# Optimization experiments

Hardware: AMD Instinct MI355X
Metric: run time of the kernel (lower is better)

Reference implementation:

```python
import jax, jax.numpy as jnp
import numpy as np

VOCAB, EMBED, HIDDEN, N_LAYER, TAG = 32000, 512, 1024, 2, 10
BATCH, MAXLEN, PAD_ID = 64, 512, 0


def setup_inputs() -> dict:
    key = jax.random.key(0)
    ks = jax.random.split(key, 12)
    x = jax.random.randint(ks[0], (BATCH, MAXLEN), 0, VOCAB, dtype=jnp.int64 if jax.config.jax_enable_x64 else jnp.int32)
    emb = jax.random.normal(ks[1], (VOCAB, EMBED), dtype=jnp.float32) * 0.02
    emb = emb.at[PAD_ID].set(0.0)  # padding_idx row zeroed
    s = 1.0 / np.sqrt(HIDDEN)
    def u(k, shape):
        return jax.random.uniform(k, shape, jnp.float32, -s, s)
    # layer 0: input EMBED -> HIDDEN; layer 1: HIDDEN -> HIDDEN. Gate order i,f,g,o.
    W_ih0 = u(ks[2], (4 * HIDDEN, EMBED))
    W_hh0 = u(ks[3], (4 * HIDDEN, HIDDEN))
    b0 = u(ks[4], (4 * HIDDEN,)) + u(ks[5], (4 * HIDDEN,))  # b_ih + b_hh fused
    W_ih1 = u(ks[6], (4 * HIDDEN, HIDDEN))
    W_hh1 = u(ks[7], (4 * HIDDEN, HIDDEN))
    b1 = u(ks[8], (4 * HIDDEN,)) + u(ks[9], (4 * HIDDEN,))
    W_out = u(ks[10], (TAG, HIDDEN))
    b_out = u(ks[11], (TAG,))
    return {"x": x, "emb": emb, "W_ih0": W_ih0, "W_hh0": W_hh0, "b0": b0,
            "W_ih1": W_ih1, "W_hh1": W_hh1, "b1": b1, "W_out": W_out, "b_out": b_out}


def lstm_layer(seq, W_ih, W_hh, b):
    # seq: [B, T, D] -> [B, T, H]
    B = seq.shape[0]
    H = W_hh.shape[1]
    x_proj = jnp.einsum('btd,gd->btg', seq, W_ih) + b  # [B, T, 4H] input projection precomputed
    x_proj = jnp.swapaxes(x_proj, 0, 1)  # [T, B, 4H]

    def step(carry, xp):
        h, c = carry
        gates = xp + h @ W_hh.T  # [B, 4H]
        i, f, g, o = jnp.split(gates, 4, axis=-1)
        c = jax.nn.sigmoid(f) * c + jax.nn.sigmoid(i) * jnp.tanh(g)
        h = jax.nn.sigmoid(o) * jnp.tanh(c)
        return (h, c), h

    init = (jnp.zeros((B, H), seq.dtype), jnp.zeros((B, H), seq.dtype))
    _, hs = jax.lax.scan(step, init, x_proj)  # hs: [T, B, H]
    return jnp.swapaxes(hs, 0, 1)


def reference(x, emb, W_ih0, W_hh0, b0, W_ih1, W_hh1, b1, W_out, b_out):
    B, T = x.shape
    lens = T - (x == PAD_ID).sum(axis=-1)  # cal_seq_len
    h = emb[x]  # [B, T, EMBED]
    h = lstm_layer(h, W_ih0, W_hh0, b0)
    h = lstm_layer(h, W_ih1, W_hh1, b1)
    last = h[jnp.arange(B), lens - 1, :]  # gather last valid hidden state
    return last @ W_out.T + b_out  # [B, TAG]
```

## Files before the change

kernel.cpp:

```cpp
#include <hip/hip_runtime.h>
#include <stdint.h>

#define BB 64
#define TT 512
#define EE 512
#define HH 1024
#define GG 4096

#define NSG 64
#define XP0_SLOTS 8

typedef short v8b __attribute__((ext_vector_type(8)));
typedef float v4f __attribute__((ext_vector_type(4)));
typedef unsigned short u16;
typedef unsigned int u32;
typedef unsigned long long u64;

__device__ __forceinline__ u16 f2bf(float f) {
  union { float f; u32 i; } v; v.f = f;
  u32 u = v.i;
  return (u16)((u + 0x7FFFu + ((u >> 16) & 1u)) >> 16);
}
__device__ __forceinline__ float sigm(float x) { return 1.0f / (1.0f + __expf(-x)); }
__device__ __forceinline__ float ftanh(float x) {
  float e = __expf(2.0f * x);
  return 1.0f - 2.0f / (e + 1.0f);
}

__device__ __forceinline__ u64 ld8a(const void* p) {
  return __hip_atomic_load((const u64*)p, __ATOMIC_RELAXED, __HIP_MEMORY_SCOPE_AGENT);
}
__device__ __forceinline__ v4f ldf16a(const float* p) {
  union { v4f f; u64 q[2]; } u;
  u.q[0] = ld8a((const u64*)p);
  u.q[1] = ld8a((const u64*)p + 1);
  return u.f;
}
__device__ __forceinline__ void stg16_f(float* p, v4f v) {
  union { v4f f; u64 q[2]; } u; u.f = v;
  __hip_atomic_store((u64*)p,     u.q[0], __ATOMIC_RELAXED, __HIP_MEMORY_SCOPE_AGENT);
  __hip_atomic_store((u64*)p + 1, u.q[1], __ATOMIC_RELAXED, __HIP_MEMORY_SCOPE_AGENT);
}
__device__ __forceinline__ void stg2_h(u16* p, u16 v) {
  __hip_atomic_store(p, v, __ATOMIC_RELAXED, __HIP_MEMORY_SCOPE_AGENT);
}
__device__ __forceinline__ void stg4_f(float* p, float v) {
  __hip_atomic_store(p, v, __ATOMIC_RELAXED, __HIP_MEMORY_SCOPE_AGENT);
}
__device__ __forceinline__ void drain_stores() {
  asm volatile("s_waitcnt vmcnt(0)" ::: "memory");
}

__device__ __forceinline__ u32 ldflag(const u32* p) {
  return __hip_atomic_load(p, __ATOMIC_RELAXED, __HIP_MEMORY_SCOPE_AGENT);
}
__device__ __forceinline__ void spin3(const u32* p0, u32 v0,
                                      const u32* p1, u32 v1,
                                      const u32* p2, u32 v2) {
  for (;;) {
    bool ok = (ldflag(p0) >= v0) && (ldflag(p1) >= v1) && (ldflag(p2) >= v2);
    if (__all((int)ok)) break;
    __builtin_amdgcn_s_sleep(1);
  }
}
__device__ __forceinline__ void postw(u32* f, u32 v, int lane) {
  if (lane == 0)
    __hip_atomic_store(f, v, __ATOMIC_RELAXED, __HIP_MEMORY_SCOPE_AGENT);
}

__global__ void prep_kernel(const int* __restrict__ x, const float* __restrict__ emb,
                            u16* __restrict__ e16, u16* __restrict__ h0r, u16* __restrict__ h1r,
                            int* __restrict__ lens, u32* flags, int flag_u32s) {
  long stride = (long)gridDim.x * blockDim.x;
  long gid = (long)blockIdx.x * blockDim.x + threadIdx.x;
  const long totalE = (long)BB * TT * EE;
  for (long i = gid; i < totalE; i += stride) {
    int d = (int)(i % EE);
    long bt = i / EE;
    int tok = x[bt];
    e16[i] = f2bf(emb[(long)tok * EE + d]);
  }
  for (long i = gid; i < (long)flag_u32s; i += stride) flags[i] = 0u;
  const long ringN = 4L * BB * HH;
  for (long i = gid; i < ringN; i += stride) { h0r[i] = 0; h1r[i] = 0; }
  int gwave = (int)(gid >> 6);
  int lane = (int)(gid & 63);
  if (gwave < BB) {
    int cnt = 0;
    for (int t2 = lane; t2 < TT; t2 += 64) cnt += (x[gwave * TT + t2] == 0) ? 1 : 0;
    for (int off = 32; off; off >>= 1) cnt += __shfl_down(cnt, off, 64);
    if (lane == 0) lens[gwave] = TT - cnt;
  }
}

extern __shared__ short Wlds[];

#define KQUAD(FR, PK) \
  { const short* wb = &Wlds[(((PK) * 4 + q) * 64 + m16) * 8]; \
    v8b w0 = *(const v8b*)(wb); \
    v8b w1 = *(const v8b*)(wb + 128); \
    v8b w2 = *(const v8b*)(wb + 256); \
    v8b w3 = *(const v8b*)(wb + 384); \
    a0 = __builtin_amdgcn_mfma_f32_16x16x32_bf16(FR, w0, a0, 0, 0, 0); \
    a1 = __builtin_amdgcn_mfma_f32_16x16x32_bf16(FR, w1, a1, 0, 0, 0); \
    a2 = __builtin_amdgcn_mfma_f32_16x16x32_bf16(FR, w2, a2, 0, 0, 0); \
    a3 = __builtin_amdgcn_mfma_f32_16x16x32_bf16(FR, w3, a3, 0, 0, 0); }

__device__ __forceinline__ void kh_staged(const u16* hbase ,
                                          int lbase ,
                                          int lane, int q, int m16,
                                          v4f& a0, v4f& a1, v4f& a2, v4f& a3) {
  const int lrow = lane >> 4;
  const int lcol = lane & 15;
  const int wG = lcol >> 1;
  const int wH = lane & 1;
  u64 hh[64];
#pragma unroll
  for (int c = 0; c < 16; ++c) {
#pragma unroll
    for (int j = 0; j < 4; ++j) {
      const u16* p = hbase + (long)(lrow + 4 * j) * HH + c * 64;
      hh[c * 4 + j] = ld8a((const u64*)p + lcol);
    }
  }
#pragma unroll
  for (int j = 0; j < 4; ++j) {
    int r = lrow + 4 * j;
    int Gs = wG ^ (r & 7);
    *(u64*)&Wlds[lbase + r * 64 + Gs * 8 + wH * 4] = hh[j];
  }
#pragma unroll
  for (int c = 0; c < 16; ++c) {
    const int boff = lbase + (c & 1) * 1024;
#pragma unroll
    for (int kb = 0; kb < 2; ++kb) {
      int Gs = (q + 4 * kb) ^ (m16 & 7);
      v8b fr = *(const v8b*)&Wlds[boff + m16 * 64 + Gs * 8];
      KQUAD(fr, c * 2 + kb);
    }
    if (c < 15) {
      const int woff = lbase + ((c + 1) & 1) * 1024;
#pragma unroll
      for (int j = 0; j < 4; ++j) {
        int r = lrow + 4 * j;
        int Gs = wG ^ (r & 7);
        *(u64*)&Wlds[woff + r * 64 + Gs * 8 + wH * 4] = hh[(c + 1) * 4 + j];
      }
    }
  }
}

__global__ __launch_bounds__(256, 1) void lstm_persist(
    const u16* __restrict__ e16,
    const float* __restrict__ Wih0, const float* __restrict__ Whh0, const float* __restrict__ b0,
    const float* __restrict__ Wih1, const float* __restrict__ Whh1, const float* __restrict__ b1,
    const int* __restrict__ lens,
    float* __restrict__ xp0, float* __restrict__ xp1,
    u16* __restrict__ h0r, u16* __restrict__ h1r,
    float* __restrict__ lasth,
    u32* fA0, u32* fL0, u32* fA1, u32* fL1) {
  const int wg = blockIdx.x;
  const int tid = threadIdx.x;
  const int g = tid >> 6;
  const int lane = tid & 63;
  const int m16 = lane & 15;
  const int q = lane >> 4;
  const int bq = g * 16 + q * 4;
  const int stage = wg >> 6;
  const int sid = wg & 63;
  const int lbase = 65536 + g * 2048;

  if (stage == 0) {
    const int rbase = sid * 64;
    for (int c2 = tid; c2 < 64 * 64; c2 += 256) {
      int r = c2 >> 6, kb = c2 & 63;
      const float* src = Wih0 + (long)(rbase + r) * EE + kb * 8;
      v8b w;
#pragma unroll
      for (int j = 0; j < 8; ++j) w[j] = (short)f2bf(src[j]);
      *(v8b*)&Wlds[(kb * 64 + r) * 8] = w;
    }
    __syncthreads();
    float bias[4];
#pragma unroll
    for (int nt = 0; nt < 4; ++nt) bias[nt] = b0[rbase + nt * 16 + m16];
    const u32* cf = fL0 + g * 64 + (sid & 15) * 4 + (lane & 3);
    u32* myf = fA0 + g * 64 + sid;
    for (int t = 0; t < TT; ++t) {
      u32 need = (t >= XP0_SLOTS) ? (u32)(t - XP0_SLOTS + 1) : 0u;
      spin3(cf, need, cf, 0u, cf, 0u);
      v4f a0 = {0,0,0,0}, a1 = {0,0,0,0}, a2 = {0,0,0,0}, a3 = {0,0,0,0};
      const u16* ap = e16 + (long)(g * 16 + m16) * (TT * EE) + (long)t * EE + q * 8;
#pragma unroll
      for (int kb = 0; kb < 16; ++kb) {
        v8b fr = *(const v8b*)(ap + kb * 32);
        KQUAD(fr, kb);
      }
      float* xpS = xp0 + (long)(t & (XP0_SLOTS - 1)) * (GG * BB);
      stg16_f(&xpS[(long)(rbase + 0 * 16 + m16) * BB + bq], a0 + bias[0]);
      stg16_f(&xpS[(long)(rbase + 1 * 16 + m16) * BB + bq], a1 + bias[1]);
      stg16_f(&xpS[(long)(rbase + 2 * 16 + m16) * BB + bq], a2 + bias[2]);
      stg16_f(&xpS[(long)(rbase + 3 * 16 + m16) * BB + bq], a3 + bias[3]);
      drain_stores();
      postw(myf, (u32)(t + 1), lane);
    }
  } else if (stage == 1) {
    const int ubase = sid * 16;
    for (int c2 = tid; c2 < 64 * 128; c2 += 256) {
      int r = c2 >> 7, kb = c2 & 127;
      int grow = (r >> 4) * HH + ubase + (r & 15);
      const float* src = Whh0 + (long)grow * HH + kb * 8;
      v8b w;
#pragma unroll
      for (int j = 0; j < 8; ++j) w[j] = (short)f2bf(src[j]);
      *(v8b*)&Wlds[(kb * 64 + r) * 8] = w;
    }
    __syncthreads();
    float cst[4] = {0.f, 0.f, 0.f, 0.f};
    const u32* fa = fA0 + g * 64 + ((lane & 3) << 4) + (sid >> 2);
    const u32* fp = fL0 + g * 64 + lane;
    const u32* fr_ = fA1 + g * 64 + lane;
    u32* myf = fL0 + g * 64 + sid;
    for (int t = 0; t < TT; ++t) {
      spin3(fa, (u32)(t + 1), fp, (u32)t, fr_, (t >= 4) ? (u32)(t - 3) : 0u);
      const float* xpS = xp0 + (long)(t & (XP0_SLOTS - 1)) * (GG * BB);
      v4f xq0 = ldf16a(&xpS[(long)(0 * HH + ubase + m16) * BB + bq]);
      v4f xq1 = ldf16a(&xpS[(long)(1 * HH + ubase + m16) * BB + bq]);
      v4f xq2 = ldf16a(&xpS[(long)(2 * HH + ubase + m16) * BB + bq]);
      v4f xq3 = ldf16a(&xpS[(long)(3 * HH + ubase + m16) * BB + bq]);
      v4f a0 = {0,0,0,0}, a1 = {0,0,0,0}, a2 = {0,0,0,0}, a3 = {0,0,0,0};
      const u16* hb = h0r + ((t + 3) & 3) * (BB * HH) + (long)(g * 16) * HH;
      kh_staged(hb, lbase, lane, q, m16, a0, a1, a2, a3);
      a0 += xq0; a1 += xq1; a2 += xq2; a3 += xq3;
      u16* hw = h0r + (t & 3) * (BB * HH);
#pragma unroll
      for (int r = 0; r < 4; ++r) {
        float cn = sigm(a1[r]) * cst[r] + sigm(a0[r]) * ftanh(a2[r]);
        cst[r] = cn;
        float hv = sigm(a3[r]) * ftanh(cn);
        stg2_h(&hw[(bq + r) * HH + ubase + m16], f2bf(hv));
      }
      drain_stores();
      postw(myf, (u32)(t + 1), lane);
    }
  } else if (stage == 2) {
    const int rbase = sid * 64;
    for (int c2 = tid; c2 < 64 * 128; c2 += 256) {
      int r = c2 >> 7, kb = c2 & 127;
      const float* src = Wih1 + (long)(rbase + r) * HH + kb * 8;
      v8b w;
#pragma unroll
      for (int j = 0; j < 8; ++j) w[j] = (short)f2bf(src[j]);
      *(v8b*)&Wlds[(kb * 64 + r) * 8] = w;
    }
    __syncthreads();
    float bias[4];
#pragma unroll
    for (int nt = 0; nt < 4; ++nt) bias[nt] = b1[rbase + nt * 16 + m16];
    const u32* fp = fL0 + g * 64 + lane;
    const u32* fc = fL1 + g * 64 + (sid & 15) * 4 + (lane & 3);
    u32* myf = fA1 + g * 64 + sid;
    for (int t = 0; t < TT; ++t) {
      spin3(fp, (u32)(t + 1), fc, (t >= 4) ? (u32)(t - 3) : 0u, fp, 0u);
      v4f a0 = {0,0,0,0}, a1 = {0,0,0,0}, a2 = {0,0,0,0}, a3 = {0,0,0,0};
      const u16* hb = h0r + (t & 3) * (BB * HH) + (long)(g * 16) * HH;
      kh_staged(hb, lbase, lane, q, m16, a0, a1, a2, a3);
      float* xpS = xp1 + (long)(t & 3) * (GG * BB);
      stg16_f(&xpS[(long)(rbase + 0 * 16 + m16) * BB + bq], a0 + bias[0]);
      stg16_f(&xpS[(long)(rbase + 1 * 16 + m16) * BB + bq], a1 + bias[1]);
      stg16_f(&xpS[(long)(rbase + 2 * 16 + m16) * BB + bq], a2 + bias[2]);
      stg16_f(&xpS[(long)(rbase + 3 * 16 + m16) * BB + bq], a3 + bias[3]);
      drain_stores();
      postw(myf, (u32)(t + 1), lane);
    }
  } else {
    const int ubase = sid * 16;
    for (int c2 = tid; c2 < 64 * 128; c2 += 256) {
      int r = c2 >> 7, kb = c2 & 127;
      int grow = (r >> 4) * HH + ubase + (r & 15);
      const float* src = Whh1 + (long)grow * HH + kb * 8;
      v8b w;
#pragma unroll
      for (int j = 0; j < 8; ++j) w[j] = (short)f2bf(src[j]);
      *(v8b*)&Wlds[(kb * 64 + r) * 8] = w;
    }
    __syncthreads();
    float cst[4] = {0.f, 0.f, 0.f, 0.f};
    int cap[4];
#pragma unroll
    for (int r = 0; r < 4; ++r) {
      int l = lens[bq + r];
      cap[r] = (l > 0) ? (l - 1) : (TT - 1);
    }
    const u32* fa = fA1 + g * 64 + ((lane & 3) << 4) + (sid >> 2);
    const u32* fp = fL1 + g * 64 + lane;
    u32* myf = fL1 + g * 64 + sid;
    for (int t = 0; t < TT; ++t) {
      spin3(fa, (u32)(t + 1), fp, (u32)t, fa, 0u);
      const float* xpS = xp1 + (long)(t & 3) * (GG * BB);
      v4f xq0 = ldf16a(&xpS[(long)(0 * HH + ubase + m16) * BB + bq]);
      v4f xq1 = ldf16a(&xpS[(long)(1 * HH + ubase + m16) * BB + bq]);
      v4f xq2 = ldf16a(&xpS[(long)(2 * HH + ubase + m16) * BB + bq]);
      v4f xq3 = ldf16a(&xpS[(long)(3 * HH + ubase + m16) * BB + bq]);
      v4f a0 = {0,0,0,0}, a1 = {0,0,0,0}, a2 = {0,0,0,0}, a3 = {0,0,0,0};
      const u16* hb = h1r + ((t + 3) & 3) * (BB * HH) + (long)(g * 16) * HH;
      kh_staged(hb, lbase, lane, q, m16, a0, a1, a2, a3);
      a0 += xq0; a1 += xq1; a2 += xq2; a3 += xq3;
      u16* hw = h1r + (t & 3) * (BB * HH);
#pragma unroll
      for (int r = 0; r < 4; ++r) {
        float cn = sigm(a1[r]) * cst[r] + sigm(a0[r]) * ftanh(a2[r]);
        cst[r] = cn;
        float hv = sigm(a3[r]) * ftanh(cn);
        stg2_h(&hw[(bq + r) * HH + ubase + m16], f2bf(hv));
        if (t == cap[r]) stg4_f(&lasth[(long)(bq + r) * HH + ubase + m16], hv);
      }
      drain_stores();
      postw(myf, (u32)(t + 1), lane);
    }
  }
}

__global__ void out_kernel(const float* __restrict__ lasth, const float* __restrict__ Wout,
                           const float* __restrict__ bout, float* __restrict__ out) {
  int b = blockIdx.x;
  int k = threadIdx.x;
  if (k < 10) {
    float acc = bout[k];
    const float* hb = lasth + (long)b * HH;
    const float* wr = Wout + (long)k * HH;
    for (int j = 0; j < HH; ++j) acc += hb[j] * wr[j];
    out[b * 10 + k] = acc;
  }
}

extern "C" void kernel_launch(void* const* d_in, const int* in_sizes, int n_in,
                              void* d_out, int out_size, void* d_ws, size_t ws_size,
                              hipStream_t stream) {
  const int*   x    = (const int*)d_in[0];
  const float* emb  = (const float*)d_in[1];
  const float* Wih0 = (const float*)d_in[2];
  const float* Whh0 = (const float*)d_in[3];
  const float* b0   = (const float*)d_in[4];
  const float* Wih1 = (const float*)d_in[5];
  const float* Whh1 = (const float*)d_in[6];
  const float* b1   = (const float*)d_in[7];
  const float* Wout = (const float*)d_in[8];
  const float* bout = (const float*)d_in[9];

  char* ws = (char*)d_ws;
  u16*   e16   = (u16*)(ws + 0);
  float* xp0   = (float*)(ws + 33554432);
  float* xp1   = (float*)(ws + 41943040);
  u16*   h0r   = (u16*)(ws + 46137344);
  u16*   h1r   = (u16*)(ws + 46661632);
  float* lasth = (float*)(ws + 47185920);
  int*   lens  = (int*)(ws + 47448064);
  u32*   flags = (u32*)(ws + 47448320);
  u32* fA0 = flags;
  u32* fL0 = fA0 + 4 * NSG;
  u32* fA1 = fL0 + 4 * NSG;
  u32* fL1 = fA1 + 4 * NSG;
  int flag_u32s = 16 * NSG;

  (void)hipFuncSetAttribute((const void*)lstm_persist,
                            hipFuncAttributeMaxDynamicSharedMemorySize, 147456);

  prep_kernel<<<2048, 256, 0, stream>>>(x, emb, e16, h0r, h1r, lens, flags, flag_u32s);
  lstm_persist<<<4 * NSG, 256, 147456, stream>>>(e16, Wih0, Whh0, b0, Wih1, Whh1, b1, lens,
                                                 xp0, xp1, h0r, h1r, lasth, fA0, fL0, fA1, fL1);
  out_kernel<<<BB, 64, 0, stream>>>(lasth, Wout, bout, (float*)d_out);
}
```

Baseline: 5.167 ms.

## Load h fragments directly into MFMA operands and pack h stores via LDS

Replaces the LDS-staged hidden-state loading (load to registers, write swizzled to LDS, read back fragments) with direct 16-byte atomic global loads into MFMA A-operands, double-buffered in two register banks of eight fragments. The 2-byte per-element h stores are replaced by an LDS exchange that packs four bf16 values into one 8-byte global store per lane. The spin-wait helpers are split by flag count so redundant flag polls are dropped, and the dynamic LDS size shrinks. This removes LDS round trips and store count on the serial recurrent critical path, at the cost of more global load traffic and register pressure.

```diff
diff --git a/kernel.cpp b/kernel.cpp
--- a/kernel.cpp
+++ b/kernel.cpp
@@ -30,6 +30,12 @@
 __device__ __forceinline__ u64 ld8a(const void* p) {
   return __hip_atomic_load((const u64*)p, __ATOMIC_RELAXED, __HIP_MEMORY_SCOPE_AGENT);
 }
+__device__ __forceinline__ v8b ld16a(const u16* p) {
+  union { v8b b; u64 q[2]; } u;
+  u.q[0] = ld8a(p);
+  u.q[1] = ld8a(p + 4);
+  return u.b;
+}
 __device__ __forceinline__ v4f ldf16a(const float* p) {
   union { v4f f; u64 q[2]; } u;
   u.q[0] = ld8a((const u64*)p);
@@ -41,8 +47,8 @@
   __hip_atomic_store((u64*)p,     u.q[0], __ATOMIC_RELAXED, __HIP_MEMORY_SCOPE_AGENT);
   __hip_atomic_store((u64*)p + 1, u.q[1], __ATOMIC_RELAXED, __HIP_MEMORY_SCOPE_AGENT);
 }
-__device__ __forceinline__ void stg2_h(u16* p, u16 v) {
-  __hip_atomic_store(p, v, __ATOMIC_RELAXED, __HIP_MEMORY_SCOPE_AGENT);
+__device__ __forceinline__ void stg8(void* p, u64 v) {
+  __hip_atomic_store((u64*)p, v, __ATOMIC_RELAXED, __HIP_MEMORY_SCOPE_AGENT);
 }
 __device__ __forceinline__ void stg4_f(float* p, float v) {
   __hip_atomic_store(p, v, __ATOMIC_RELAXED, __HIP_MEMORY_SCOPE_AGENT);
@@ -50,15 +56,38 @@
 __device__ __forceinline__ void drain_stores() {
   asm volatile("s_waitcnt vmcnt(0)" ::: "memory");
 }
+__device__ __forceinline__ void lds_fence() {
+  asm volatile("s_waitcnt lgkmcnt(0)" ::: "memory");
+}
 
 __device__ __forceinline__ u32 ldflag(const u32* p) {
   return __hip_atomic_load(p, __ATOMIC_RELAXED, __HIP_MEMORY_SCOPE_AGENT);
 }
-__device__ __forceinline__ void spin3(const u32* p0, u32 v0,
-                                      const u32* p1, u32 v1,
-                                      const u32* p2, u32 v2) {
+__device__ __forceinline__ void spin1p(const u32* p0, u32 v0) {
   for (;;) {
-    bool ok = (ldflag(p0) >= v0) && (ldflag(p1) >= v1) && (ldflag(p2) >= v2);
+    u32 a = ldflag(p0);
+    if (__all((int)(a >= v0))) break;
+    __builtin_amdgcn_s_sleep(1);
+  }
+}
+__device__ __forceinline__ void spin2p(const u32* p0, u32 v0,
+                                       const u32* p1, u32 v1) {
+  for (;;) {
+    u32 a = ldflag(p0);
+    u32 b = ldflag(p1);
+    bool ok = (a >= v0) & (b >= v1);
+    if (__all((int)ok)) break;
+    __builtin_amdgcn_s_sleep(1);
+  }
+}
+__device__ __forceinline__ void spin3p(const u32* p0, u32 v0,
+                                       const u32* p1, u32 v1,
+                                       const u32* p2, u32 v2) {
+  for (;;) {
+    u32 a = ldflag(p0);
+    u32 b = ldflag(p1);
+    u32 c = ldflag(p2);
+    bool ok = (a >= v0) & (b >= v1) & (c >= v2);
     if (__all((int)ok)) break;
     __builtin_amdgcn_s_sleep(1);
   }
@@ -106,48 +135,25 @@
     a2 = __builtin_amdgcn_mfma_f32_16x16x32_bf16(FR, w2, a2, 0, 0, 0); \
     a3 = __builtin_amdgcn_mfma_f32_16x16x32_bf16(FR, w3, a3, 0, 0, 0); }
 
-__device__ __forceinline__ void kh_staged(const u16* hbase ,
-                                          int lbase ,
-                                          int lane, int q, int m16,
-                                          v4f& a0, v4f& a1, v4f& a2, v4f& a3) {
-  const int lrow = lane >> 4;
-  const int lcol = lane & 15;
-  const int wG = lcol >> 1;
-  const int wH = lane & 1;
-  u64 hh[64];
-#pragma unroll
-  for (int c = 0; c < 16; ++c) {
-#pragma unroll
-    for (int j = 0; j < 4; ++j) {
-      const u16* p = hbase + (long)(lrow + 4 * j) * HH + c * 64;
-      hh[c * 4 + j] = ld8a((const u64*)p + lcol);
-    }
-  }
-#pragma unroll
-  for (int j = 0; j < 4; ++j) {
-    int r = lrow + 4 * j;
-    int Gs = wG ^ (r & 7);
-    *(u64*)&Wlds[lbase + r * 64 + Gs * 8 + wH * 4] = hh[j];
-  }
-#pragma unroll
-  for (int c = 0; c < 16; ++c) {
-    const int boff = lbase + (c & 1) * 1024;
-#pragma unroll
-    for (int kb = 0; kb < 2; ++kb) {
-      int Gs = (q + 4 * kb) ^ (m16 & 7);
-      v8b fr = *(const v8b*)&Wlds[boff + m16 * 64 + Gs * 8];
-      KQUAD(fr, c * 2 + kb);
-    }
-    if (c < 15) {
-      const int woff = lbase + ((c + 1) & 1) * 1024;
-#pragma unroll
-      for (int j = 0; j < 4; ++j) {
-        int r = lrow + 4 * j;
-        int Gs = wG ^ (r & 7);
-        *(u64*)&Wlds[woff + r * 64 + Gs * 8 + wH * 4] = hh[(c + 1) * 4 + j];
-      }
-    }
-  }
+__device__ __forceinline__ void khloop(const u16* hp, int q, int m16,
+                                       v4f& a0, v4f& a1, v4f& a2, v4f& a3) {
+  v8b A[8], B[8];
+#pragma unroll
+  for (int i = 0; i < 8; ++i) A[i] = ld16a(hp + i * 32);
+#pragma unroll
+  for (int i = 0; i < 8; ++i) B[i] = ld16a(hp + (8 + i) * 32);
+#pragma unroll
+  for (int i = 0; i < 8; ++i) KQUAD(A[i], i);
+#pragma unroll
+  for (int i = 0; i < 8; ++i) A[i] = ld16a(hp + (16 + i) * 32);
+#pragma unroll
+  for (int i = 0; i < 8; ++i) KQUAD(B[i], 8 + i);
+#pragma unroll
+  for (int i = 0; i < 8; ++i) B[i] = ld16a(hp + (24 + i) * 32);
+#pragma unroll
+  for (int i = 0; i < 8; ++i) KQUAD(A[i], 16 + i);
+#pragma unroll
+  for (int i = 0; i < 8; ++i) KQUAD(B[i], 24 + i);
 }
 
 __global__ __launch_bounds__(256, 1) void lstm_persist(
@@ -168,7 +174,7 @@
   const int bq = g * 16 + q * 4;
   const int stage = wg >> 6;
   const int sid = wg & 63;
-  const int lbase = 65536 + g * 2048;
+  const int exbase = 65536 + g * 256;
 
   if (stage == 0) {
     const int rbase = sid * 64;
@@ -187,8 +193,7 @@
     const u32* cf = fL0 + g * 64 + (sid & 15) * 4 + (lane & 3);
     u32* myf = fA0 + g * 64 + sid;
     for (int t = 0; t < TT; ++t) {
-      u32 need = (t >= XP0_SLOTS) ? (u32)(t - XP0_SLOTS + 1) : 0u;
-      spin3(cf, need, cf, 0u, cf, 0u);
+      if (t >= XP0_SLOTS) spin1p(cf, (u32)(t - XP0_SLOTS + 1));
       v4f a0 = {0,0,0,0}, a1 = {0,0,0,0}, a2 = {0,0,0,0}, a3 = {0,0,0,0};
       const u16* ap = e16 + (long)(g * 16 + m16) * (TT * EE) + (long)t * EE + q * 8;
 #pragma unroll
@@ -221,25 +226,30 @@
     const u32* fp = fL0 + g * 64 + lane;
     const u32* fr_ = fA1 + g * 64 + lane;
     u32* myf = fL0 + g * 64 + sid;
+    short* ex = &Wlds[exbase];
+    const int bl = lane >> 2, qa = lane & 3;
     for (int t = 0; t < TT; ++t) {
-      spin3(fa, (u32)(t + 1), fp, (u32)t, fr_, (t >= 4) ? (u32)(t - 3) : 0u);
+      spin3p(fa, (u32)(t + 1), fp, (u32)t, fr_, (t >= 4) ? (u32)(t - 3) : 0u);
       const float* xpS = xp0 + (long)(t & (XP0_SLOTS - 1)) * (GG * BB);
       v4f xq0 = ldf16a(&xpS[(long)(0 * HH + ubase + m16) * BB + bq]);
       v4f xq1 = ldf16a(&xpS[(long)(1 * HH + ubase + m16) * BB + bq]);
       v4f xq2 = ldf16a(&xpS[(long)(2 * HH + ubase + m16) * BB + bq]);
       v4f xq3 = ldf16a(&xpS[(long)(3 * HH + ubase + m16) * BB + bq]);
       v4f a0 = {0,0,0,0}, a1 = {0,0,0,0}, a2 = {0,0,0,0}, a3 = {0,0,0,0};
-      const u16* hb = h0r + ((t + 3) & 3) * (BB * HH) + (long)(g * 16) * HH;
-      kh_staged(hb, lbase, lane, q, m16, a0, a1, a2, a3);
+      const u16* hp = h0r + ((t + 3) & 3) * (BB * HH) + (long)(g * 16 + m16) * HH + q * 8;
+      khloop(hp, q, m16, a0, a1, a2, a3);
       a0 += xq0; a1 += xq1; a2 += xq2; a3 += xq3;
-      u16* hw = h0r + (t & 3) * (BB * HH);
 #pragma unroll
       for (int r = 0; r < 4; ++r) {
         float cn = sigm(a1[r]) * cst[r] + sigm(a0[r]) * ftanh(a2[r]);
         cst[r] = cn;
         float hv = sigm(a3[r]) * ftanh(cn);
-        stg2_h(&hw[(bq + r) * HH + ubase + m16], f2bf(hv));
+        ex[(q * 4 + r) * 16 + m16] = (short)f2bf(hv);
       }
+      lds_fence();
+      u16* hw = h0r + (t & 3) * (BB * HH);
+      u64 pk = *(const u64*)&ex[bl * 16 + qa * 4];
+      stg8(&hw[(long)(g * 16 + bl) * HH + ubase + qa * 4], pk);
       drain_stores();
       postw(myf, (u32)(t + 1), lane);
     }
@@ -261,10 +271,10 @@
     const u32* fc = fL1 + g * 64 + (sid & 15) * 4 + (lane & 3);
     u32* myf = fA1 + g * 64 + sid;
     for (int t = 0; t < TT; ++t) {
-      spin3(fp, (u32)(t + 1), fc, (t >= 4) ? (u32)(t - 3) : 0u, fp, 0u);
+      spin2p(fp, (u32)(t + 1), fc, (t >= 4) ? (u32)(t - 3) : 0u);
       v4f a0 = {0,0,0,0}, a1 = {0,0,0,0}, a2 = {0,0,0,0}, a3 = {0,0,0,0};
-      const u16* hb = h0r + (t & 3) * (BB * HH) + (long)(g * 16) * HH;
-      kh_staged(hb, lbase, lane, q, m16, a0, a1, a2, a3);
+      const u16* hp = h0r + (t & 3) * (BB * HH) + (long)(g * 16 + m16) * HH + q * 8;
+      khloop(hp, q, m16, a0, a1, a2, a3);
       float* xpS = xp1 + (long)(t & 3) * (GG * BB);
       stg16_f(&xpS[(long)(rbase + 0 * 16 + m16) * BB + bq], a0 + bias[0]);
       stg16_f(&xpS[(long)(rbase + 1 * 16 + m16) * BB + bq], a1 + bias[1]);
@@ -295,26 +305,31 @@
     const u32* fa = fA1 + g * 64 + ((lane & 3) << 4) + (sid >> 2);
     const u32* fp = fL1 + g * 64 + lane;
     u32* myf = fL1 + g * 64 + sid;
+    short* ex = &Wlds[exbase];
+    const int bl = lane >> 2, qa = lane & 3;
     for (int t = 0; t < TT; ++t) {
-      spin3(fa, (u32)(t + 1), fp, (u32)t, fa, 0u);
+      spin2p(fa, (u32)(t + 1), fp, (u32)t);
       const float* xpS = xp1 + (long)(t & 3) * (GG * BB);
       v4f xq0 = ldf16a(&xpS[(long)(0 * HH + ubase + m16) * BB + bq]);
       v4f xq1 = ldf16a(&xpS[(long)(1 * HH + ubase + m16) * BB + bq]);
       v4f xq2 = ldf16a(&xpS[(long)(2 * HH + ubase + m16) * BB + bq]);
       v4f xq3 = ldf16a(&xpS[(long)(3 * HH + ubase + m16) * BB + bq]);
       v4f a0 = {0,0,0,0}, a1 = {0,0,0,0}, a2 = {0,0,0,0}, a3 = {0,0,0,0};
-      const u16* hb = h1r + ((t + 3) & 3) * (BB * HH) + (long)(g * 16) * HH;
-      kh_staged(hb, lbase, lane, q, m16, a0, a1, a2, a3);
+      const u16* hp = h1r + ((t + 3) & 3) * (BB * HH) + (long)(g * 16 + m16) * HH + q * 8;
+      khloop(hp, q, m16, a0, a1, a2, a3);
       a0 += xq0; a1 += xq1; a2 += xq2; a3 += xq3;
-      u16* hw = h1r + (t & 3) * (BB * HH);
 #pragma unroll
       for (int r = 0; r < 4; ++r) {
         float cn = sigm(a1[r]) * cst[r] + sigm(a0[r]) * ftanh(a2[r]);
         cst[r] = cn;
         float hv = sigm(a3[r]) * ftanh(cn);
-        stg2_h(&hw[(bq + r) * HH + ubase + m16], f2bf(hv));
+        ex[(q * 4 + r) * 16 + m16] = (short)f2bf(hv);
         if (t == cap[r]) stg4_f(&lasth[(long)(bq + r) * HH + ubase + m16], hv);
       }
+      lds_fence();
+      u16* hw = h1r + (t & 3) * (BB * HH);
+      u64 pk = *(const u64*)&ex[bl * 16 + qa * 4];
+      stg8(&hw[(long)(g * 16 + bl) * HH + ubase + qa * 4], pk);
       drain_stores();
       postw(myf, (u32)(t + 1), lane);
     }
@@ -364,10 +379,10 @@
   int flag_u32s = 16 * NSG;
 
   (void)hipFuncSetAttribute((const void*)lstm_persist,
-                            hipFuncAttributeMaxDynamicSharedMemorySize, 147456);
+                            hipFuncAttributeMaxDynamicSharedMemorySize, 133120);
 
   prep_kernel<<<2048, 256, 0, stream>>>(x, emb, e16, h0r, h1r, lens, flags, flag_u32s);
-  lstm_persist<<<4 * NSG, 256, 147456, stream>>>(e16, Wih0, Whh0, b0, Wih1, Whh1, b1, lens,
+  lstm_persist<<<4 * NSG, 256, 133120, stream>>>(e16, Wih0, Whh0, b0, Wih1, Whh1, b1, lens,
                                                  xp0, xp1, h0r, h1r, lasth, fA0, fL0, fA1, fL1);
   out_kernel<<<BB, 64, 0, stream>>>(lasth, Wout, bout, (float*)d_out);
 }
```

Result: slower. 8.781 ms (+69.9%).

## Load recurrent h fragments directly from global, drop LDS staging, deepen rings

Applied to the files above, without the earlier changes.

Replaces the LDS-staged hidden-state load, which did coalesced 8-byte atomic loads, swizzled writes to shared memory and then read MFMA fragments back, with 16-byte global loads using sc0 sc1 cache bits that go straight into MFMA operand registers. The xproj loads use the same instruction. The h and xp1 ring buffers grow from 4 to 8 slots so producer stages can run further ahead, and the stage-0 spin is skipped for the first slots. This removes LDS traffic and per-step staging latency in the serial recurrence, at the cost of less coalesced global loads, higher register pressure (32 v8b fragments), and relying on inline-asm cache bits for cross-workgroup coherence.

```diff
diff --git a/kernel.cpp b/kernel.cpp
--- a/kernel.cpp
+++ b/kernel.cpp
@@ -9,6 +9,7 @@
 
 #define NSG 64
 #define XP0_SLOTS 8
+#define RS 8
 
 typedef short v8b __attribute__((ext_vector_type(8)));
 typedef float v4f __attribute__((ext_vector_type(4)));
@@ -27,15 +28,21 @@
   return 1.0f - 2.0f / (e + 1.0f);
 }
 
-__device__ __forceinline__ u64 ld8a(const void* p) {
-  return __hip_atomic_load((const u64*)p, __ATOMIC_RELAXED, __HIP_MEMORY_SCOPE_AGENT);
-}
-__device__ __forceinline__ v4f ldf16a(const float* p) {
-  union { v4f f; u64 q[2]; } u;
-  u.q[0] = ld8a((const u64*)p);
-  u.q[1] = ld8a((const u64*)p + 1);
-  return u.f;
-}
+__device__ __forceinline__ v8b ld16cc(const u16* p) {
+  v8b r;
+  asm volatile("global_load_dwordx4 %0, %1, off sc0 sc1" : "=v"(r) : "v"(p));
+  return r;
+}
+__device__ __forceinline__ v4f ldf16cc(const float* p) {
+  v4f r;
+  asm volatile("global_load_dwordx4 %0, %1, off sc0 sc1" : "=v"(r) : "v"(p));
+  return r;
+}
+__device__ __forceinline__ void wait_loads() {
+  asm volatile("s_waitcnt vmcnt(0)" ::: "memory");
+  __builtin_amdgcn_sched_barrier(0);
+}
+
 __device__ __forceinline__ void stg16_f(float* p, v4f v) {
   union { v4f f; u64 q[2]; } u; u.f = v;
   __hip_atomic_store((u64*)p,     u.q[0], __ATOMIC_RELAXED, __HIP_MEMORY_SCOPE_AGENT);
@@ -81,7 +88,7 @@
     e16[i] = f2bf(emb[(long)tok * EE + d]);
   }
   for (long i = gid; i < (long)flag_u32s; i += stride) flags[i] = 0u;
-  const long ringN = 4L * BB * HH;
+  const long ringN = (long)RS * BB * HH;
   for (long i = gid; i < ringN; i += stride) { h0r[i] = 0; h1r[i] = 0; }
   int gwave = (int)(gid >> 6);
   int lane = (int)(gid & 63);
@@ -106,48 +113,16 @@
     a2 = __builtin_amdgcn_mfma_f32_16x16x32_bf16(FR, w2, a2, 0, 0, 0); \
     a3 = __builtin_amdgcn_mfma_f32_16x16x32_bf16(FR, w3, a3, 0, 0, 0); }
 
-__device__ __forceinline__ void kh_staged(const u16* hbase ,
-                                          int lbase ,
-                                          int lane, int q, int m16,
+__device__ __forceinline__ void kh_direct(const u16* hbase ,
+                                          int q, int m16,
                                           v4f& a0, v4f& a1, v4f& a2, v4f& a3) {
-  const int lrow = lane >> 4;
-  const int lcol = lane & 15;
-  const int wG = lcol >> 1;
-  const int wH = lane & 1;
-  u64 hh[64];
-#pragma unroll
-  for (int c = 0; c < 16; ++c) {
-#pragma unroll
-    for (int j = 0; j < 4; ++j) {
-      const u16* p = hbase + (long)(lrow + 4 * j) * HH + c * 64;
-      hh[c * 4 + j] = ld8a((const u64*)p + lcol);
-    }
-  }
-#pragma unroll
-  for (int j = 0; j < 4; ++j) {
-    int r = lrow + 4 * j;
-    int Gs = wG ^ (r & 7);
-    *(u64*)&Wlds[lbase + r * 64 + Gs * 8 + wH * 4] = hh[j];
-  }
-#pragma unroll
-  for (int c = 0; c < 16; ++c) {
-    const int boff = lbase + (c & 1) * 1024;
-#pragma unroll
-    for (int kb = 0; kb < 2; ++kb) {
-      int Gs = (q + 4 * kb) ^ (m16 & 7);
-      v8b fr = *(const v8b*)&Wlds[boff + m16 * 64 + Gs * 8];
-      KQUAD(fr, c * 2 + kb);
-    }
-    if (c < 15) {
-      const int woff = lbase + ((c + 1) & 1) * 1024;
-#pragma unroll
-      for (int j = 0; j < 4; ++j) {
-        int r = lrow + 4 * j;
-        int Gs = wG ^ (r & 7);
-        *(u64*)&Wlds[woff + r * 64 + Gs * 8 + wH * 4] = hh[(c + 1) * 4 + j];
-      }
-    }
-  }
+  const u16* hp = hbase + (long)m16 * HH + q * 8;
+  v8b H[32];
+#pragma unroll
+  for (int kb = 0; kb < 32; ++kb) H[kb] = ld16cc(hp + kb * 32);
+  wait_loads();
+#pragma unroll
+  for (int kb = 0; kb < 32; ++kb) KQUAD(H[kb], kb);
 }
 
 __global__ __launch_bounds__(256, 1) void lstm_persist(
@@ -168,7 +143,6 @@
   const int bq = g * 16 + q * 4;
   const int stage = wg >> 6;
   const int sid = wg & 63;
-  const int lbase = 65536 + g * 2048;
 
   if (stage == 0) {
     const int rbase = sid * 64;
@@ -187,8 +161,7 @@
     const u32* cf = fL0 + g * 64 + (sid & 15) * 4 + (lane & 3);
     u32* myf = fA0 + g * 64 + sid;
     for (int t = 0; t < TT; ++t) {
-      u32 need = (t >= XP0_SLOTS) ? (u32)(t - XP0_SLOTS + 1) : 0u;
-      spin3(cf, need, cf, 0u, cf, 0u);
+      if (t >= XP0_SLOTS) spin3(cf, (u32)(t - XP0_SLOTS + 1), cf, 0u, cf, 0u);
       v4f a0 = {0,0,0,0}, a1 = {0,0,0,0}, a2 = {0,0,0,0}, a3 = {0,0,0,0};
       const u16* ap = e16 + (long)(g * 16 + m16) * (TT * EE) + (long)t * EE + q * 8;
 #pragma unroll
@@ -222,17 +195,17 @@
     const u32* fr_ = fA1 + g * 64 + lane;
     u32* myf = fL0 + g * 64 + sid;
     for (int t = 0; t < TT; ++t) {
-      spin3(fa, (u32)(t + 1), fp, (u32)t, fr_, (t >= 4) ? (u32)(t - 3) : 0u);
+      spin3(fa, (u32)(t + 1), fp, (u32)t, fr_, (t >= RS) ? (u32)(t - RS + 1) : 0u);
       const float* xpS = xp0 + (long)(t & (XP0_SLOTS - 1)) * (GG * BB);
-      v4f xq0 = ldf16a(&xpS[(long)(0 * HH + ubase + m16) * BB + bq]);
-      v4f xq1 = ldf16a(&xpS[(long)(1 * HH + ubase + m16) * BB + bq]);
-      v4f xq2 = ldf16a(&xpS[(long)(2 * HH + ubase + m16) * BB + bq]);
-      v4f xq3 = ldf16a(&xpS[(long)(3 * HH + ubase + m16) * BB + bq]);
+      v4f xq0 = ldf16cc(&xpS[(long)(0 * HH + ubase + m16) * BB + bq]);
+      v4f xq1 = ldf16cc(&xpS[(long)(1 * HH + ubase + m16) * BB + bq]);
+      v4f xq2 = ldf16cc(&xpS[(long)(2 * HH + ubase + m16) * BB + bq]);
+      v4f xq3 = ldf16cc(&xpS[(long)(3 * HH + ubase + m16) * BB + bq]);
       v4f a0 = {0,0,0,0}, a1 = {0,0,0,0}, a2 = {0,0,0,0}, a3 = {0,0,0,0};
-      const u16* hb = h0r + ((t + 3) & 3) * (BB * HH) + (long)(g * 16) * HH;
-      kh_staged(hb, lbase, lane, q, m16, a0, a1, a2, a3);
+      const u16* hb = h0r + ((t + RS - 1) & (RS - 1)) * (BB * HH) + (long)(g * 16) * HH;
+      kh_direct(hb, q, m16, a0, a1, a2, a3);
       a0 += xq0; a1 += xq1; a2 += xq2; a3 += xq3;
-      u16* hw = h0r + (t & 3) * (BB * HH);
+      u16* hw = h0r + (t & (RS - 1)) * (BB * HH);
 #pragma unroll
       for (int r = 0; r < 4; ++r) {
         float cn = sigm(a1[r]) * cst[r] + sigm(a0[r]) * ftanh(a2[r]);
@@ -261,11 +234,11 @@
     const u32* fc = fL1 + g * 64 + (sid & 15) * 4 + (lane & 3);
     u32* myf = fA1 + g * 64 + sid;
     for (int t = 0; t < TT; ++t) {
-      spin3(fp, (u32)(t + 1), fc, (t >= 4) ? (u32)(t - 3) : 0u, fp, 0u);
+      spin3(fp, (u32)(t + 1), fc, (t >= RS) ? (u32)(t - RS + 1) : 0u, fp, 0u);
       v4f a0 = {0,0,0,0}, a1 = {0,0,0,0}, a2 = {0,0,0,0}, a3 = {0,0,0,0};
-      const u16* hb = h0r + (t & 3) * (BB * HH) + (long)(g * 16) * HH;
-      kh_staged(hb, lbase, lane, q, m16, a0, a1, a2, a3);
-      float* xpS = xp1 + (long)(t & 3) * (GG * BB);
+      const u16* hb = h0r + (t & (RS - 1)) * (BB * HH) + (long)(g * 16) * HH;
+      kh_direct(hb, q, m16, a0, a1, a2, a3);
+      float* xpS = xp1 + (long)(t & (RS - 1)) * (GG * BB);
       stg16_f(&xpS[(long)(rbase + 0 * 16 + m16) * BB + bq], a0 + bias[0]);
       stg16_f(&xpS[(long)(rbase + 1 * 16 + m16) * BB + bq], a1 + bias[1]);
       stg16_f(&xpS[(long)(rbase + 2 * 16 + m16) * BB + bq], a2 + bias[2]);
@@ -297,16 +270,16 @@
     u32* myf = fL1 + g * 64 + sid;
     for (int t = 0; t < TT; ++t) {
       spin3(fa, (u32)(t + 1), fp, (u32)t, fa, 0u);
-      const float* xpS = xp1 + (long)(t & 3) * (GG * BB);
-      v4f xq0 = ldf16a(&xpS[(long)(0 * HH + ubase + m16) * BB + bq]);
-      v4f xq1 = ldf16a(&xpS[(long)(1 * HH + ubase + m16) * BB + bq]);
-      v4f xq2 = ldf16a(&xpS[(long)(2 * HH + ubase + m16) * BB + bq]);
-      v4f xq3 = ldf16a(&xpS[(long)(3 * HH + ubase + m16) * BB + bq]);
+      const float* xpS = xp1 + (long)(t & (RS - 1)) * (GG * BB);
+      v4f xq0 = ldf16cc(&xpS[(long)(0 * HH + ubase + m16) * BB + bq]);
+      v4f xq1 = ldf16cc(&xpS[(long)(1 * HH + ubase + m16) * BB + bq]);
+      v4f xq2 = ldf16cc(&xpS[(long)(2 * HH + ubase + m16) * BB + bq]);
+      v4f xq3 = ldf16cc(&xpS[(long)(3 * HH + ubase + m16) * BB + bq]);
       v4f a0 = {0,0,0,0}, a1 = {0,0,0,0}, a2 = {0,0,0,0}, a3 = {0,0,0,0};
-      const u16* hb = h1r + ((t + 3) & 3) * (BB * HH) + (long)(g * 16) * HH;
-      kh_staged(hb, lbase, lane, q, m16, a0, a1, a2, a3);
+      const u16* hb = h1r + ((t + RS - 1) & (RS - 1)) * (BB * HH) + (long)(g * 16) * HH;
+      kh_direct(hb, q, m16, a0, a1, a2, a3);
       a0 += xq0; a1 += xq1; a2 += xq2; a3 += xq3;
-      u16* hw = h1r + (t & 3) * (BB * HH);
+      u16* hw = h1r + (t & (RS - 1)) * (BB * HH);
 #pragma unroll
       for (int r = 0; r < 4; ++r) {
         float cn = sigm(a1[r]) * cst[r] + sigm(a0[r]) * ftanh(a2[r]);
@@ -352,11 +325,11 @@
   u16*   e16   = (u16*)(ws + 0);
   float* xp0   = (float*)(ws + 33554432);
   float* xp1   = (float*)(ws + 41943040);
-  u16*   h0r   = (u16*)(ws + 46137344);
-  u16*   h1r   = (u16*)(ws + 46661632);
-  float* lasth = (float*)(ws + 47185920);
-  int*   lens  = (int*)(ws + 47448064);
-  u32*   flags = (u32*)(ws + 47448320);
+  u16*   h0r   = (u16*)(ws + 50331648);
+  u16*   h1r   = (u16*)(ws + 51380224);
+  float* lasth = (float*)(ws + 52428800);
+  int*   lens  = (int*)(ws + 52690944);
+  u32*   flags = (u32*)(ws + 52691200);
   u32* fA0 = flags;
   u32* fL0 = fA0 + 4 * NSG;
   u32* fA1 = fL0 + 4 * NSG;
@@ -364,10 +337,10 @@
   int flag_u32s = 16 * NSG;
 
   (void)hipFuncSetAttribute((const void*)lstm_persist,
-                            hipFuncAttributeMaxDynamicSharedMemorySize, 147456);
+                            hipFuncAttributeMaxDynamicSharedMemorySize, 131072);
 
   prep_kernel<<<2048, 256, 0, stream>>>(x, emb, e16, h0r, h1r, lens, flags, flag_u32s);
-  lstm_persist<<<4 * NSG, 256, 147456, stream>>>(e16, Wih0, Whh0, b0, Wih1, Whh1, b1, lens,
+  lstm_persist<<<4 * NSG, 256, 131072, stream>>>(e16, Wih0, Whh0, b0, Wih1, Whh1, b1, lens,
                                                  xp0, xp1, h0r, h1r, lasth, fA0, fL0, fA1, fL1);
   out_kernel<<<BB, 64, 0, stream>>>(lasth, Wout, bout, (float*)d_out);
 }
```

After: 6.449 ms. 24.8% more time.

## Deepen LSTM hidden-state rings to 8 slots and batch cross-stage flag waits

Applied to the files above, without the earlier changes.

Enlarges the h0/h1 and xp1 ring buffers from 4 to 8 slots and moves the workspace offsets to fit them. With the extra slack, the slack-side producer/consumer flags are checked only every fourth timestep with a lookahead of four steps, instead of on every step. Only the tight recurrence dependency is still waited on each step, which cuts flag polling and the coupling between pipeline stages. The cost is more workspace and more ring memory to initialise, and the batched waits need exact ring-slack arithmetic to avoid overwrite races.

```diff
diff --git a/kernel.cpp b/kernel.cpp
--- a/kernel.cpp
+++ b/kernel.cpp
@@ -9,6 +9,7 @@
 
 #define NSG 64
 #define XP0_SLOTS 8
+#define RS 8
 
 typedef short v8b __attribute__((ext_vector_type(8)));
 typedef float v4f __attribute__((ext_vector_type(4)));
@@ -53,6 +54,21 @@
 
 __device__ __forceinline__ u32 ldflag(const u32* p) {
   return __hip_atomic_load(p, __ATOMIC_RELAXED, __HIP_MEMORY_SCOPE_AGENT);
+}
+__device__ __forceinline__ void spin1(const u32* p0, u32 v0) {
+  for (;;) {
+    bool ok = (ldflag(p0) >= v0);
+    if (__all((int)ok)) break;
+    __builtin_amdgcn_s_sleep(1);
+  }
+}
+__device__ __forceinline__ void spin2(const u32* p0, u32 v0,
+                                      const u32* p1, u32 v1) {
+  for (;;) {
+    bool ok = (ldflag(p0) >= v0) && (ldflag(p1) >= v1);
+    if (__all((int)ok)) break;
+    __builtin_amdgcn_s_sleep(1);
+  }
 }
 __device__ __forceinline__ void spin3(const u32* p0, u32 v0,
                                       const u32* p1, u32 v1,
@@ -81,7 +97,7 @@
     e16[i] = f2bf(emb[(long)tok * EE + d]);
   }
   for (long i = gid; i < (long)flag_u32s; i += stride) flags[i] = 0u;
-  const long ringN = 4L * BB * HH;
+  const long ringN = (long)RS * BB * HH;
   for (long i = gid; i < ringN; i += stride) { h0r[i] = 0; h1r[i] = 0; }
   int gwave = (int)(gid >> 6);
   int lane = (int)(gid & 63);
@@ -187,8 +203,7 @@
     const u32* cf = fL0 + g * 64 + (sid & 15) * 4 + (lane & 3);
     u32* myf = fA0 + g * 64 + sid;
     for (int t = 0; t < TT; ++t) {
-      u32 need = (t >= XP0_SLOTS) ? (u32)(t - XP0_SLOTS + 1) : 0u;
-      spin3(cf, need, cf, 0u, cf, 0u);
+      if ((t & 3) == 0 && t >= 8) spin1(cf, (u32)(t - 4));
       v4f a0 = {0,0,0,0}, a1 = {0,0,0,0}, a2 = {0,0,0,0}, a3 = {0,0,0,0};
       const u16* ap = e16 + (long)(g * 16 + m16) * (TT * EE) + (long)t * EE + q * 8;
 #pragma unroll
@@ -222,17 +237,23 @@
     const u32* fr_ = fA1 + g * 64 + lane;
     u32* myf = fL0 + g * 64 + sid;
     for (int t = 0; t < TT; ++t) {
-      spin3(fa, (u32)(t + 1), fp, (u32)t, fr_, (t >= 4) ? (u32)(t - 3) : 0u);
+      if ((t & 3) == 0) {
+        u32 va = (u32)((t + 4 < TT) ? t + 4 : TT);
+        u32 vr = (t >= 8) ? (u32)(t - 4) : 0u;
+        spin3(fa, va, fp, (u32)t, fr_, vr);
+      } else {
+        spin1(fp, (u32)t);
+      }
       const float* xpS = xp0 + (long)(t & (XP0_SLOTS - 1)) * (GG * BB);
       v4f xq0 = ldf16a(&xpS[(long)(0 * HH + ubase + m16) * BB + bq]);
       v4f xq1 = ldf16a(&xpS[(long)(1 * HH + ubase + m16) * BB + bq]);
       v4f xq2 = ldf16a(&xpS[(long)(2 * HH + ubase + m16) * BB + bq]);
       v4f xq3 = ldf16a(&xpS[(long)(3 * HH + ubase + m16) * BB + bq]);
       v4f a0 = {0,0,0,0}, a1 = {0,0,0,0}, a2 = {0,0,0,0}, a3 = {0,0,0,0};
-      const u16* hb = h0r + ((t + 3) & 3) * (BB * HH) + (long)(g * 16) * HH;
+      const u16* hb = h0r + ((t + RS - 1) & (RS - 1)) * (BB * HH) + (long)(g * 16) * HH;
       kh_staged(hb, lbase, lane, q, m16, a0, a1, a2, a3);
       a0 += xq0; a1 += xq1; a2 += xq2; a3 += xq3;
-      u16* hw = h0r + (t & 3) * (BB * HH);
+      u16* hw = h0r + (t & (RS - 1)) * (BB * HH);
 #pragma unroll
       for (int r = 0; r < 4; ++r) {
         float cn = sigm(a1[r]) * cst[r] + sigm(a0[r]) * ftanh(a2[r]);
@@ -261,11 +282,16 @@
     const u32* fc = fL1 + g * 64 + (sid & 15) * 4 + (lane & 3);
     u32* myf = fA1 + g * 64 + sid;
     for (int t = 0; t < TT; ++t) {
-      spin3(fp, (u32)(t + 1), fc, (t >= 4) ? (u32)(t - 3) : 0u, fp, 0u);
+      if ((t & 3) == 0) {
+        u32 vc = (t >= 8) ? (u32)(t - 4) : 0u;
+        spin2(fp, (u32)(t + 1), fc, vc);
+      } else {
+        spin1(fp, (u32)(t + 1));
+      }
       v4f a0 = {0,0,0,0}, a1 = {0,0,0,0}, a2 = {0,0,0,0}, a3 = {0,0,0,0};
-      const u16* hb = h0r + (t & 3) * (BB * HH) + (long)(g * 16) * HH;
+      const u16* hb = h0r + (t & (RS - 1)) * (BB * HH) + (long)(g * 16) * HH;
       kh_staged(hb, lbase, lane, q, m16, a0, a1, a2, a3);
-      float* xpS = xp1 + (long)(t & 3) * (GG * BB);
+      float* xpS = xp1 + (long)(t & (RS - 1)) * (GG * BB);
       stg16_f(&xpS[(long)(rbase + 0 * 16 + m16) * BB + bq], a0 + bias[0]);
       stg16_f(&xpS[(long)(rbase + 1 * 16 + m16) * BB + bq], a1 + bias[1]);
       stg16_f(&xpS[(long)(rbase + 2 * 16 + m16) * BB + bq], a2 + bias[2]);
@@ -296,17 +322,17 @@
     const u32* fp = fL1 + g * 64 + lane;
     u32* myf = fL1 + g * 64 + sid;
     for (int t = 0; t < TT; ++t) {
-      spin3(fa, (u32)(t + 1), fp, (u32)t, fa, 0u);
-      const float* xpS = xp1 + (long)(t & 3) * (GG * BB);
+      spin2(fa, (u32)(t + 1), fp, (u32)t);
+      const float* xpS = xp1 + (long)(t & (RS - 1)) * (GG * BB);
       v4f xq0 = ldf16a(&xpS[(long)(0 * HH + ubase + m16) * BB + bq]);
       v4f xq1 = ldf16a(&xpS[(long)(1 * HH + ubase + m16) * BB + bq]);
       v4f xq2 = ldf16a(&xpS[(long)(2 * HH + ubase + m16) * BB + bq]);
       v4f xq3 = ldf16a(&xpS[(long)(3 * HH + ubase + m16) * BB + bq]);
       v4f a0 = {0,0,0,0}, a1 = {0,0,0,0}, a2 = {0,0,0,0}, a3 = {0,0,0,0};
-      const u16* hb = h1r + ((t + 3) & 3) * (BB * HH) + (long)(g * 16) * HH;
+      const u16* hb = h1r + ((t + RS - 1) & (RS - 1)) * (BB * HH) + (long)(g * 16) * HH;
       kh_staged(hb, lbase, lane, q, m16, a0, a1, a2, a3);
       a0 += xq0; a1 += xq1; a2 += xq2; a3 += xq3;
-      u16* hw = h1r + (t & 3) * (BB * HH);
+      u16* hw = h1r + (t & (RS - 1)) * (BB * HH);
 #pragma unroll
       for (int r = 0; r < 4; ++r) {
         float cn = sigm(a1[r]) * cst[r] + sigm(a0[r]) * ftanh(a2[r]);
@@ -352,11 +378,11 @@
   u16*   e16   = (u16*)(ws + 0);
   float* xp0   = (float*)(ws + 33554432);
   float* xp1   = (float*)(ws + 41943040);
-  u16*   h0r   = (u16*)(ws + 46137344);
-  u16*   h1r   = (u16*)(ws + 46661632);
-  float* lasth = (float*)(ws + 47185920);
-  int*   lens  = (int*)(ws + 47448064);
-  u32*   flags = (u32*)(ws + 47448320);
+  u16*   h0r   = (u16*)(ws + 50331648);
+  u16*   h1r   = (u16*)(ws + 51380224);
+  float* lasth = (float*)(ws + 52428800);
+  int*   lens  = (int*)(ws + 52690944);
+  u32*   flags = (u32*)(ws + 52691200);
   u32* fA0 = flags;
   u32* fL0 = fA0 + 4 * NSG;
   u32* fA1 = fL0 + 4 * NSG;
```

Measured after the change: 5.557 ms. +7.5%, slower.
